# Kernel tuning notes

Hardware: AMD Instinct MI355X
Metric: run time of the kernel (lower is better)

## Reference

```python
import jax, jax.numpy as jnp
import numpy as np

N_NODES = 100_000
N_EDGES = 1_600_000
NFEAT = 16          # nfeature_dim
HID = 128           # hidden_dim
K = 3               # TAGConv hops in pretrained convs
N_LAYERS = 4        # pretrained n_gnn_layers (1 in->hid + 3 hid->hid)
OUT_DIM = 1


def _gcn_norm(edge_index, n):
    # PyG TAGConv: symmetric gcn_norm WITHOUT self-loops (k=0 term covers self).
    row, col = edge_index[0], edge_index[1]
    deg = jax.ops.segment_sum(jnp.ones((edge_index.shape[1],), jnp.float32), col, num_segments=n)
    dis = jnp.where(deg > 0, jax.lax.rsqrt(jnp.maximum(deg, 1.0)), 0.0)
    return dis[row] * dis[col]


def _tagconv(x, row, col, norm, ws, b, n):
    # out = sum_k (A_hat^k x) W_k + b ; ws: [K+1, in, out]
    out = x @ ws[0]
    h = x
    for k in range(1, ws.shape[0]):
        h = jax.ops.segment_sum(h[row] * norm[:, None], col, num_segments=n)
        out = out + h @ ws[k]
    return out + b


def setup_inputs() -> dict:
    key = jax.random.key(0)
    ks = jax.random.split(key, 10)
    x = jax.random.normal(ks[0], (N_NODES, NFEAT + 1), jnp.float32)
    edge_index = jax.random.randint(ks[1], (2, N_EDGES), 0, N_NODES, dtype=jnp.int64)
    # featureEmbedding: TAGConv(17 -> 16, K=1) -> 2 weight mats + bias
    fe_ws = jax.random.normal(ks[2], (2, NFEAT + 1, NFEAT), jnp.float32) * (NFEAT + 1) ** -0.5
    fe_b = jnp.zeros((NFEAT,), jnp.float32)
    # convs[0]: TAGConv(16 -> 128, K=3)
    conv0_ws = jax.random.normal(ks[3], (K + 1, NFEAT, HID), jnp.float32) * NFEAT ** -0.5
    conv0_b = jnp.zeros((HID,), jnp.float32)
    # convs[1..3]: TAGConv(128 -> 128, K=3), stacked
    conv_ws = jax.random.normal(ks[4], (N_LAYERS - 1, K + 1, HID, HID), jnp.float32) * HID ** -0.5
    conv_b = jnp.zeros((N_LAYERS - 1, HID), jnp.float32)
    fc_w = jax.random.normal(ks[5], (HID, OUT_DIM), jnp.float32) * HID ** -0.5
    fc_b = jnp.zeros((OUT_DIM,), jnp.float32)
    return {"x": x, "edge_index": edge_index, "fe_ws": fe_ws, "fe_b": fe_b,
            "conv0_ws": conv0_ws, "conv0_b": conv0_b,
            "conv_ws": conv_ws, "conv_b": conv_b, "fc_w": fc_w, "fc_b": fc_b}


def reference(x, edge_index, fe_ws, fe_b, conv0_ws, conv0_b, conv_ws, conv_b, fc_w, fc_b):
    n = x.shape[0]
    row, col = edge_index[0], edge_index[1]
    norm = _gcn_norm(edge_index, n)
    # featureEmbedding (K=1)
    h = _tagconv(x, row, col, norm, fe_ws, fe_b, n)
    # convs[0..n-2] with dropout (eval-mode identity) + ReLU
    h = _tagconv(h, row, col, norm, conv0_ws, conv0_b, n)
    h = jax.nn.relu(h)
    for i in range(conv_ws.shape[0] - 1):
        h = _tagconv(h, row, col, norm, conv_ws[i], conv_b[i], n)
        h = jax.nn.relu(h)
    # last conv: no dropout/relu
    h = _tagconv(h, row, col, norm, conv_ws[-1], conv_b[-1], n)
    return h @ fc_w + fc_b
```

## Files before the change

### kernel.cpp

```cpp
#include <hip/hip_runtime.h>

#define NN 100000
#define NE 1600000
#define SCAN_B 98
#define NB 782
#define SUBCAP 512
#define MAXB 4096

typedef _Float16 half8 __attribute__((ext_vector_type(8)));
typedef float f32x4 __attribute__((ext_vector_type(4)));
struct h2s { _Float16 x, y; };
struct h4s { _Float16 a, b, c, d; };

__global__ void k_deg(const int* __restrict__ col, int* __restrict__ degi) {
  int e = blockIdx.x * blockDim.x + threadIdx.x;
  if (e < NE) atomicAdd(&degi[col[e]], 1);
}

__global__ void k_dis(const int* __restrict__ degi, float* __restrict__ dis) {
  int i = blockIdx.x * blockDim.x + threadIdx.x;
  if (i < NN) {
    int d = degi[i];
    dis[i] = d > 0 ? rsqrtf((float)d) : 0.0f;
  }
}

__global__ void k_scan1(const int* __restrict__ degi, int* __restrict__ bsum) {
  __shared__ int red[256];
  int t = threadIdx.x;
  int base = blockIdx.x * 1024 + t * 4;
  int s = 0;
#pragma unroll
  for (int u = 0; u < 4; ++u) {
    int i = base + u;
    if (i < NN) s += degi[i];
  }
  red[t] = s;
  __syncthreads();
  for (int o = 128; o; o >>= 1) {
    if (t < o) red[t] += red[t + o];
    __syncthreads();
  }
  if (t == 0) bsum[blockIdx.x] = red[0];
}

__global__ void k_scan2(const int* __restrict__ bsum, int* __restrict__ boff,
                        int* __restrict__ off) {
  __shared__ int sh[128];
  int t = threadIdx.x;
  int v = (t < SCAN_B) ? bsum[t] : 0;
  sh[t] = v;
  __syncthreads();
  for (int o = 1; o < 128; o <<= 1) {
    int u = (t >= o) ? sh[t - o] : 0;
    __syncthreads();
    sh[t] += u;
    __syncthreads();
  }
  if (t < SCAN_B) boff[t] = sh[t] - v;
  if (t == 127) off[NN] = sh[127];
}

__global__ void k_scan3(const int* __restrict__ degi, const int* __restrict__ boff,
                        int* __restrict__ off) {
  __shared__ int red[256];
  int t = threadIdx.x;
  int base = blockIdx.x * 1024 + t * 4;
  int d[4];
  int s = 0;
#pragma unroll
  for (int u = 0; u < 4; ++u) {
    int i = base + u;
    d[u] = (i < NN) ? degi[i] : 0;
    s += d[u];
  }
  red[t] = s;
  __syncthreads();
  for (int o = 1; o < 256; o <<= 1) {
    int u2 = (t >= o) ? red[t - o] : 0;
    __syncthreads();
    red[t] += u2;
    __syncthreads();
  }
  int pre = red[t] - s + boff[blockIdx.x];
#pragma unroll
  for (int u = 0; u < 4; ++u) {
    int i = base + u;
    if (i < NN) {
      off[i] = pre;
      pre += d[u];
    }
  }
}

__global__ void k_bscatter(const int* __restrict__ row, const int* __restrict__ col,
                           int* __restrict__ bcur, unsigned* __restrict__ pk2) {
  int e = blockIdx.x * blockDim.x + threadIdx.x;
  int x = blockIdx.x & 7;
  if (e < NE) {
    int c = col[e];
    int cell = ((c >> 7) << 3) | x;
    int slot = atomicAdd(&bcur[cell * 16], 1);
    slot = min(slot, SUBCAP - 1);
    pk2[(size_t)cell * SUBCAP + slot] = (unsigned)row[e] | ((unsigned)(c & 127) << 17);
  }
}

__global__ __launch_bounds__(256) void k_bsort(const unsigned* __restrict__ pk2,
                                               const int* __restrict__ bcur,
                                               const int* __restrict__ off,
                                               const float* __restrict__ dis,
                                               int* __restrict__ src,
                                               _Float16* __restrict__ wh) {
  __shared__ unsigned epk[MAXB];
  __shared__ int cnt[128];
  __shared__ int sc[128];
  __shared__ int cur[128];
  __shared__ float sdis[128];
  __shared__ int soff[9];
  int b = blockIdx.x;
  int n0 = b << 7;
  int gb = off[n0];
  int t = threadIdx.x;
  if (t == 0) {
    int acc = 0;
#pragma unroll
    for (int x = 0; x < 8; ++x) {
      soff[x] = acc;
      acc += min(bcur[((b << 3) | x) * 16], SUBCAP);
    }
    soff[8] = acc;
  }
  if (t < 128) {
    cnt[t] = 0;
    sdis[t] = (n0 + t < NN) ? dis[n0 + t] : 0.f;
  }
  __syncthreads();
  int m = soff[8];
#pragma unroll
  for (int x = 0; x < 8; ++x) {
    int c0 = soff[x], c1 = soff[x + 1];
    const unsigned* seg = &pk2[(size_t)((b << 3) | x) * SUBCAP];
    for (int i = c0 + t; i < c1; i += 256) epk[i] = seg[i - c0];
  }
  __syncthreads();
  for (int i = t; i < m; i += 256) atomicAdd(&cnt[epk[i] >> 17], 1);
  __syncthreads();
  if (t < 128) sc[t] = cnt[t];
  __syncthreads();
  for (int o = 1; o < 128; o <<= 1) {
    int u = (t < 128 && t >= o) ? sc[t - o] : 0;
    __syncthreads();
    if (t < 128) sc[t] += u;
    __syncthreads();
  }
  if (t < 128) cur[t] = sc[t] - cnt[t];
  __syncthreads();
  for (int i = t; i < m; i += 256) {
    unsigned p = epk[i];
    int c = (int)(p >> 17);
    int r = (int)(p & 0x1FFFFu);
    int pos = gb + atomicAdd(&cur[c], 1);
    src[pos] = r;
    wh[pos] = (_Float16)(dis[r] * sdis[c]);
  }
}

__global__ void k_wprep(const float* __restrict__ cw, _Float16* __restrict__ wt) {
  int i = blockIdx.x * 256 + threadIdx.x;
  if (i < 12 * 16384) {
    int mat = i >> 14;
    int rem = i & 16383;
    int k = rem >> 7;
    int n = rem & 127;
    wt[(mat << 14) | (n << 7) | k] = (_Float16)cw[i];
  }
}

__global__ void k_uprep(const float* __restrict__ cw, const float* __restrict__ cb,
                        const float* __restrict__ fcw, const float* __restrict__ fcb,
                        float* __restrict__ uvec, float* __restrict__ cval) {
  int i = blockIdx.x * 256 + threadIdx.x;
  if (i < 512) {
    int s = i >> 7, k = i & 127;
    const float* W = cw + (size_t)(8 + s) * 16384 + k * 128;
    float acc = 0.f;
    for (int n = 0; n < 128; ++n) acc += W[n] * fcw[n];
    uvec[i] = acc;
  }
  if (i == 512) {
    float acc = 0.f;
    for (int n = 0; n < 128; ++n) acc += cb[2 * 128 + n] * fcw[n];
    *cval = acc + fcb[0];
  }
}

__global__ void k_prop16h(const h2s* __restrict__ h, const int* __restrict__ off,
                          const int* __restrict__ src, const _Float16* __restrict__ wh,
                          h2s* __restrict__ out) {
  int t = threadIdx.x;
  int node = blockIdx.x * 8 + (t >> 3);
  int f = t & 7;
  int b = off[node], e = off[node + 1];
  float ax = 0.f, ay = 0.f;
  int j = b;
  for (; j + 2 <= e; j += 2) {
    int s0 = src[j], s1 = src[j + 1];
    float w0 = (float)wh[j], w1 = (float)wh[j + 1];
    h2s v0 = h[s0 * 8 + f];
    h2s v1 = h[s1 * 8 + f];
    ax = fmaf((float)v0.x, w0, fmaf((float)v1.x, w1, ax));
    ay = fmaf((float)v0.y, w0, fmaf((float)v1.y, w1, ay));
  }
  if (j < e) {
    int s = src[j];
    float w = (float)wh[j];
    h2s v = h[s * 8 + f];
    ax = fmaf((float)v.x, w, ax);
    ay = fmaf((float)v.y, w, ay);
  }
  h2s o;
  o.x = (_Float16)ax;
  o.y = (_Float16)ay;
  unsigned bits;
  __builtin_memcpy(&bits, &o, 4);
  __builtin_nontemporal_store(bits, (unsigned*)&out[node * 8 + f]);
}

__global__ void k_prop128h(const h2s* __restrict__ h, const int* __restrict__ off,
                           const int* __restrict__ src, const _Float16* __restrict__ wh,
                           h2s* __restrict__ out) {
  int node = blockIdx.x;
  int t = threadIdx.x;
  int b = off[node], e = off[node + 1];
  float ax = 0.f, ay = 0.f;
  int j = b;
  for (; j + 8 <= e; j += 8) {
    h2s v[8];
    float w[8];
#pragma unroll
    for (int u = 0; u < 8; ++u) {
      v[u] = h[src[j + u] * 64 + t];
      w[u] = (float)wh[j + u];
    }
#pragma unroll
    for (int u = 0; u < 8; ++u) {
      ax = fmaf((float)v[u].x, w[u], ax);
      ay = fmaf((float)v[u].y, w[u], ay);
    }
  }
  for (; j < e; ++j) {
    int s = src[j];
    float w = (float)wh[j];
    h2s v = h[s * 64 + t];
    ax = fmaf((float)v.x, w, ax);
    ay = fmaf((float)v.y, w, ay);
  }
  h2s o;
  o.x = (_Float16)ax;
  o.y = (_Float16)ay;
  unsigned bits;
  __builtin_memcpy(&bits, &o, 4);
  __builtin_nontemporal_store(bits, (unsigned*)&out[node * 64 + t]);
}

template <bool RELU>
__global__ __launch_bounds__(256) void k_tag4_mfma(
    const _Float16* __restrict__ A0, const _Float16* __restrict__ A1,
    const _Float16* __restrict__ A2, const _Float16* __restrict__ A3,
    const _Float16* __restrict__ Wt, const float* __restrict__ bias,
    _Float16* __restrict__ out) {
  __shared__ _Float16 Wl[16384];
  int tid = threadIdx.x;
  int wid = tid >> 6;
  int lane = tid & 63;
  int r = lane & 15, kg = lane >> 4;
  int m0 = blockIdx.x * 128 + wid * 32;
  int row0 = min(m0 + r, NN - 1);
  int row1 = min(m0 + 16 + r, NN - 1);
  f32x4 acc0[8] = {}, acc1[8] = {};
  const _Float16* As[4] = {A0, A1, A2, A3};
#pragma unroll
  for (int s = 0; s < 4; ++s) {
    const float4* Wg = (const float4*)(Wt + (s << 14));
    __syncthreads();
#pragma unroll
    for (int u = 0; u < 8; ++u) {
      int g = tid + u * 256;
      int sg = g ^ ((g >> 4) & 7);
      *(float4*)((char*)Wl + g * 16) = Wg[sg];
    }
    __syncthreads();
    const _Float16* A = As[s];
    half8 a0[4], a1[4];
#pragma unroll
    for (int kc = 0; kc < 4; ++kc) {
      int kbase = kc * 32 + kg * 8;
      a0[kc] = *(const half8*)&A[(size_t)row0 * 128 + kbase];
      a1[kc] = *(const half8*)&A[(size_t)row1 * 128 + kbase];
    }
#pragma unroll
    for (int kc = 0; kc < 4; ++kc) {
      int kb2 = (kc * 32 + kg * 8) * 2;
#pragma unroll
      for (int nb = 0; nb < 8; ++nb) {
        int n = nb * 16 + r;
        int ba = ((n << 8) + kb2) ^ ((n & 7) << 4);
        half8 b = *(const half8*)((const char*)Wl + ba);
        acc0[nb] = __builtin_amdgcn_mfma_f32_16x16x32_f16(a0[kc], b, acc0[nb], 0, 0, 0);
        acc1[nb] = __builtin_amdgcn_mfma_f32_16x16x32_f16(a1[kc], b, acc1[nb], 0, 0, 0);
      }
    }
  }
  int ccol = lane & 15;
#pragma unroll
  for (int h = 0; h < 2; ++h) {
    int crow0 = m0 + h * 16 + kg * 4;
#pragma unroll
    for (int nb = 0; nb < 8; ++nb) {
      int col = nb * 16 + ccol;
      float bv = bias[col];
      const f32x4& av = h ? acc1[nb] : acc0[nb];
#pragma unroll
      for (int e = 0; e < 4; ++e) {
        float v = av[e] + bv;
        if (RELU) v = fmaxf(v, 0.f);
        int rr = crow0 + e;
        if (rr < NN) out[(size_t)rr * 128 + col] = (_Float16)v;
      }
    }
  }
}

__global__ void k_tagfc(const _Float16* __restrict__ A0, const _Float16* __restrict__ A1,
                        const _Float16* __restrict__ A2, const _Float16* __restrict__ A3,
                        const float* __restrict__ uvec, const float* __restrict__ cval,
                        float* __restrict__ out) {
  int node = blockIdx.x;
  int t = threadIdx.x;
  const h2s* As[4] = {(const h2s*)A0, (const h2s*)A1, (const h2s*)A2, (const h2s*)A3};
  float s = 0.f;
#pragma unroll
  for (int q = 0; q < 4; ++q) {
    h2s v = As[q][(size_t)node * 64 + t];
    float2 u = ((const float2*)(uvec + (q << 7)))[t];
    s = fmaf((float)v.x, u.x, fmaf((float)v.y, u.y, s));
  }
  for (int o = 32; o; o >>= 1) s += __shfl_down(s, o);
  if (t == 0) out[node] = s + *cval;
}

__global__ __launch_bounds__(256) void k_conv0_fused(
    const _Float16* __restrict__ A0, const _Float16* __restrict__ A1,
    const _Float16* __restrict__ A2, const _Float16* __restrict__ A3,
    const float* __restrict__ W , const float* __restrict__ bias,
    _Float16* __restrict__ out) {
  __shared__ float Wl[4 * 16 * 128];
  for (int i = threadIdx.x * 4; i < 4 * 16 * 128; i += 1024)
    *(float4*)&Wl[i] = *(const float4*)&W[i];
  __syncthreads();
  int r0 = blockIdx.x * 32 + (threadIdx.x >> 5) * 4;
  int c0 = (threadIdx.x & 31) * 4;
  float acc[4][4] = {};
  const _Float16* As[4] = {A0, A1, A2, A3};
#pragma unroll
  for (int s = 0; s < 4; ++s) {
    const _Float16* A = As[s];
    const float* Ws = &Wl[s * 2048];
#pragma unroll
    for (int k = 0; k < 16; k += 4) {
      float4 w0 = *(const float4*)&Ws[(k + 0) * 128 + c0];
      float4 w1 = *(const float4*)&Ws[(k + 1) * 128 + c0];
      float4 w2 = *(const float4*)&Ws[(k + 2) * 128 + c0];
      float4 w3 = *(const float4*)&Ws[(k + 3) * 128 + c0];
#pragma unroll
      for (int i = 0; i < 4; ++i) {
        h4s a4 = *(const h4s*)&A[(r0 + i) * 16 + k];
        float ax = (float)a4.a, ay = (float)a4.b, az = (float)a4.c, aw = (float)a4.d;
        acc[i][0] = fmaf(ax, w0.x, fmaf(ay, w1.x, fmaf(az, w2.x, fmaf(aw, w3.x, acc[i][0]))));
        acc[i][1] = fmaf(ax, w0.y, fmaf(ay, w1.y, fmaf(az, w2.y, fmaf(aw, w3.y, acc[i][1]))));
        acc[i][2] = fmaf(ax, w0.z, fmaf(ay, w1.z, fmaf(az, w2.z, fmaf(aw, w3.z, acc[i][2]))));
        acc[i][3] = fmaf(ax, w0.w, fmaf(ay, w1.w, fmaf(az, w2.w, fmaf(aw, w3.w, acc[i][3]))));
      }
    }
  }
#pragma unroll
  for (int i = 0; i < 4; ++i) {
    h4s o;
    o.a = (_Float16)fmaxf(acc[i][0] + bias[c0 + 0], 0.f);
    o.b = (_Float16)fmaxf(acc[i][1] + bias[c0 + 1], 0.f);
    o.c = (_Float16)fmaxf(acc[i][2] + bias[c0 + 2], 0.f);
    o.d = (_Float16)fmaxf(acc[i][3] + bias[c0 + 3], 0.f);
    *(h4s*)&out[(size_t)(r0 + i) * 128 + c0] = o;
  }
}

template <int IN, bool ACCUM, bool BIAS>
__global__ void k_mm16h(const float* __restrict__ A, const float* __restrict__ W,
                        const float* __restrict__ bias, _Float16* __restrict__ C) {
  __shared__ float Wl[IN * 16];
  for (int i = threadIdx.x; i < IN * 16; i += 256) Wl[i] = W[i];
  __syncthreads();
  int r = blockIdx.x * 16 + (threadIdx.x >> 4);
  int c = threadIdx.x & 15;
  float acc = 0.f;
  for (int k = 0; k < IN; ++k) acc += A[r * IN + k] * Wl[k * 16 + c];
  int idx = r * 16 + c;
  if (BIAS) acc += bias[c];
  if (ACCUM) acc += (float)C[idx];
  C[idx] = (_Float16)acc;
}

extern "C" void kernel_launch(void* const* d_in, const int* in_sizes, int n_in,
                              void* d_out, int out_size, void* d_ws, size_t ws_size,
                              hipStream_t stream) {
  const float* x = (const float*)d_in[0];
  const int* ei = (const int*)d_in[1];
  const float* fe_ws = (const float*)d_in[2];
  const float* fe_b = (const float*)d_in[3];
  const float* c0_ws = (const float*)d_in[4];
  const float* c0_b = (const float*)d_in[5];
  const float* cw = (const float*)d_in[6];
  const float* cb = (const float*)d_in[7];
  const float* fcw = (const float*)d_in[8];
  const float* fcb = (const float*)d_in[9];
  float* out = (float*)d_out;

  const int* row = ei;
  const int* colv = ei + NE;

  char* wp = (char*)d_ws;
  auto alloc = [&](size_t bytes) {
    char* p = wp;
    wp += (bytes + 511) & ~(size_t)511;
    return p;
  };
  int* degi = (int*)alloc(NN * 4);
  int* off = (int*)alloc((NN + 1) * 4);
  int* bsum = (int*)alloc(SCAN_B * 4);
  int* boff = (int*)alloc(SCAN_B * 4);
  int* bcur = (int*)alloc((size_t)NB * 8 * 16 * 4);
  float* dis = (float*)alloc(NN * 4);
  int* src = (int*)alloc((size_t)NE * 4);
  unsigned* pk2 = (unsigned*)alloc((size_t)NB * 8 * SUBCAP * 4);
  _Float16* wh = (_Float16*)alloc((size_t)NE * 2);
  _Float16* wsT = (_Float16*)alloc((size_t)12 * 16384 * 2);
  float* uvec = (float*)alloc(512 * 4);
  float* cval = (float*)alloc(4);
  _Float16* y1h = (_Float16*)alloc((size_t)NN * 16 * 2);
  _Float16* h16 = (_Float16*)alloc((size_t)NN * 16 * 2);
  _Float16* p16b = (_Float16*)alloc((size_t)NN * 16 * 2);
  _Float16* p16c = (_Float16*)alloc((size_t)NN * 16 * 2);
  _Float16* p16d = (_Float16*)alloc((size_t)NN * 16 * 2);
  _Float16* H0 = (_Float16*)alloc((size_t)NN * 128 * 2);
  _Float16* H1 = (_Float16*)alloc((size_t)NN * 128 * 2);
  _Float16* T1 = (_Float16*)alloc((size_t)NN * 128 * 2);
  _Float16* T2 = (_Float16*)alloc((size_t)NN * 128 * 2);
  _Float16* T3 = (_Float16*)alloc((size_t)NN * 128 * 2);

  hipMemsetAsync(degi, 0, NN * 4, stream);
  hipMemsetAsync(bcur, 0, (size_t)NB * 8 * 16 * 4, stream);
  k_deg<<<(NE + 255) / 256, 256, 0, stream>>>(colv, degi);
  k_dis<<<(NN + 255) / 256, 256, 0, stream>>>(degi, dis);
  k_scan1<<<SCAN_B, 256, 0, stream>>>(degi, bsum);
  k_scan2<<<1, 128, 0, stream>>>(bsum, boff, off);
  k_scan3<<<SCAN_B, 256, 0, stream>>>(degi, boff, off);
  k_bscatter<<<(NE + 255) / 256, 256, 0, stream>>>(row, colv, bcur, pk2);
  k_bsort<<<NB, 256, 0, stream>>>(pk2, bcur, off, dis, src, wh);
  k_wprep<<<768, 256, 0, stream>>>(cw, wsT);
  k_uprep<<<3, 256, 0, stream>>>(cw, cb, fcw, fcb, uvec, cval);

  k_mm16h<17, false, false><<<NN / 16, 256, 0, stream>>>(x, fe_ws + 17 * 16, nullptr, y1h);
  k_prop16h<<<NN / 8, 64, 0, stream>>>((const h2s*)y1h, off, src, wh, (h2s*)h16);
  k_mm16h<17, true, true><<<NN / 16, 256, 0, stream>>>(x, fe_ws, fe_b, h16);

  k_prop16h<<<NN / 8, 64, 0, stream>>>((const h2s*)h16, off, src, wh, (h2s*)p16b);
  k_prop16h<<<NN / 8, 64, 0, stream>>>((const h2s*)p16b, off, src, wh, (h2s*)p16c);
  k_prop16h<<<NN / 8, 64, 0, stream>>>((const h2s*)p16c, off, src, wh, (h2s*)p16d);
  k_conv0_fused<<<NN / 32, 256, 0, stream>>>(h16, p16b, p16c, p16d, c0_ws, c0_b, H0);

  _Float16* hin = H0;
  _Float16* hout = H1;
  int mgrid = (NN + 127) / 128;
  for (int l = 0; l < 2; ++l) {
    k_prop128h<<<NN, 64, 0, stream>>>((const h2s*)hin, off, src, wh, (h2s*)T1);
    k_prop128h<<<NN, 64, 0, stream>>>((const h2s*)T1, off, src, wh, (h2s*)T2);
    k_prop128h<<<NN, 64, 0, stream>>>((const h2s*)T2, off, src, wh, (h2s*)T3);
    const _Float16* Wl = wsT + (size_t)l * 4 * 16384;
    const float* bl = cb + l * 128;
    k_tag4_mfma<true><<<mgrid, 256, 0, stream>>>(hin, T1, T2, T3, Wl, bl, hout);
    _Float16* t = hin; hin = hout; hout = t;
  }

  k_prop128h<<<NN, 64, 0, stream>>>((const h2s*)hin, off, src, wh, (h2s*)T1);
  k_prop128h<<<NN, 64, 0, stream>>>((const h2s*)T1, off, src, wh, (h2s*)T2);
  k_prop128h<<<NN, 64, 0, stream>>>((const h2s*)T2, off, src, wh, (h2s*)T3);
  k_tagfc<<<NN, 64, 0, stream>>>(hin, T1, T2, T3, uvec, cval, out);
}
```

Measured before the change: 942.3 us.

## Pack edge source and weight into one 64-bit record, shuffle-broadcast in propagation

Replaces the separate src (int) and fp16 weight arrays with one 64-bit array holding the source index and an fp32 weight. In the 128-wide propagation kernel, each group of 8 lanes loads one packed record and broadcasts it with a shuffle, instead of every lane reading the index and weight separately. That kernel also moves from one 64-thread block per node to four nodes per 256-thread block, and bscatter uses a nontemporal store. This cuts scalar index loads and block-launch overhead, at the cost of more edge bytes (8 instead of 6 per edge) and added shuffle instructions.

Result: slower. 1.067 ms (+13.2%).

```diff
diff --git a/kernel.cpp b/kernel.cpp
--- a/kernel.cpp
+++ b/kernel.cpp
@@ -11,6 +11,12 @@
 typedef float f32x4 __attribute__((ext_vector_type(4)));
 struct h2s { _Float16 x, y; };
 struct h4s { _Float16 a, b, c, d; };
+
+static __device__ __forceinline__ void unpack_pair(long pv, int& s, float& w) {
+  s = (int)(unsigned int)(pv & 0xffffffffL);
+  int wi = (int)(pv >> 32);
+  __builtin_memcpy(&w, &wi, 4);
+}
 
 __global__ void k_deg(const int* __restrict__ col, int* __restrict__ degi) {
   int e = blockIdx.x * blockDim.x + threadIdx.x;
@@ -102,7 +108,8 @@
     int cell = ((c >> 7) << 3) | x;
     int slot = atomicAdd(&bcur[cell * 16], 1);
     slot = min(slot, SUBCAP - 1);
-    pk2[(size_t)cell * SUBCAP + slot] = (unsigned)row[e] | ((unsigned)(c & 127) << 17);
+    unsigned v = (unsigned)row[e] | ((unsigned)(c & 127) << 17);
+    __builtin_nontemporal_store(v, &pk2[(size_t)cell * SUBCAP + slot]);
   }
 }
 
@@ -110,8 +117,7 @@
                                                const int* __restrict__ bcur,
                                                const int* __restrict__ off,
                                                const float* __restrict__ dis,
-                                               int* __restrict__ src,
-                                               _Float16* __restrict__ wh) {
+                                               long* __restrict__ E) {
   __shared__ unsigned epk[MAXB];
   __shared__ int cnt[128];
   __shared__ int sc[128];
@@ -161,8 +167,10 @@
     int c = (int)(p >> 17);
     int r = (int)(p & 0x1FFFFu);
     int pos = gb + atomicAdd(&cur[c], 1);
-    src[pos] = r;
-    wh[pos] = (_Float16)(dis[r] * sdis[c]);
+    float w = dis[r] * sdis[c];
+    int wi;
+    __builtin_memcpy(&wi, &w, 4);
+    E[pos] = (long)(unsigned int)r | ((long)wi << 32);
   }
 }
 
@@ -196,8 +204,7 @@
 }
 
 __global__ void k_prop16h(const h2s* __restrict__ h, const int* __restrict__ off,
-                          const int* __restrict__ src, const _Float16* __restrict__ wh,
-                          h2s* __restrict__ out) {
+                          const long* __restrict__ E, h2s* __restrict__ out) {
   int t = threadIdx.x;
   int node = blockIdx.x * 8 + (t >> 3);
   int f = t & 7;
@@ -205,16 +212,19 @@
   float ax = 0.f, ay = 0.f;
   int j = b;
   for (; j + 2 <= e; j += 2) {
-    int s0 = src[j], s1 = src[j + 1];
-    float w0 = (float)wh[j], w1 = (float)wh[j + 1];
+    int s0, s1;
+    float w0, w1;
+    unpack_pair(E[j], s0, w0);
+    unpack_pair(E[j + 1], s1, w1);
     h2s v0 = h[s0 * 8 + f];
     h2s v1 = h[s1 * 8 + f];
     ax = fmaf((float)v0.x, w0, fmaf((float)v1.x, w1, ax));
     ay = fmaf((float)v0.y, w0, fmaf((float)v1.y, w1, ay));
   }
   if (j < e) {
-    int s = src[j];
-    float w = (float)wh[j];
+    int s;
+    float w;
+    unpack_pair(E[j], s, w);
     h2s v = h[s * 8 + f];
     ax = fmaf((float)v.x, w, ax);
     ay = fmaf((float)v.y, w, ay);
@@ -227,21 +237,25 @@
   __builtin_nontemporal_store(bits, (unsigned*)&out[node * 8 + f]);
 }
 
-__global__ void k_prop128h(const h2s* __restrict__ h, const int* __restrict__ off,
-                           const int* __restrict__ src, const _Float16* __restrict__ wh,
-                           h2s* __restrict__ out) {
-  int node = blockIdx.x;
-  int t = threadIdx.x;
+__global__ __launch_bounds__(256) void k_prop128h(const h2s* __restrict__ h,
+                                                  const int* __restrict__ off,
+                                                  const long* __restrict__ E,
+                                                  h2s* __restrict__ out) {
+  int node = blockIdx.x * 4 + (threadIdx.x >> 6);
+  int t = threadIdx.x & 63;
   int b = off[node], e = off[node + 1];
   float ax = 0.f, ay = 0.f;
   int j = b;
   for (; j + 8 <= e; j += 8) {
+    long pv = E[j + (t & 7)];
     h2s v[8];
     float w[8];
 #pragma unroll
     for (int u = 0; u < 8; ++u) {
-      v[u] = h[src[j + u] * 64 + t];
-      w[u] = (float)wh[j + u];
+      long p = __shfl(pv, u, 8);
+      int s;
+      unpack_pair(p, s, w[u]);
+      v[u] = h[s * 64 + t];
     }
 #pragma unroll
     for (int u = 0; u < 8; ++u) {
@@ -250,8 +264,9 @@
     }
   }
   for (; j < e; ++j) {
-    int s = src[j];
-    float w = (float)wh[j];
+    int s;
+    float w;
+    unpack_pair(E[j], s, w);
     h2s v = h[s * 64 + t];
     ax = fmaf((float)v.x, w, ax);
     ay = fmaf((float)v.y, w, ay);
@@ -441,9 +456,8 @@
   int* boff = (int*)alloc(SCAN_B * 4);
   int* bcur = (int*)alloc((size_t)NB * 8 * 16 * 4);
   float* dis = (float*)alloc(NN * 4);
-  int* src = (int*)alloc((size_t)NE * 4);
+  long* E = (long*)alloc((size_t)NE * 8);
   unsigned* pk2 = (unsigned*)alloc((size_t)NB * 8 * SUBCAP * 4);
-  _Float16* wh = (_Float16*)alloc((size_t)NE * 2);
   _Float16* wsT = (_Float16*)alloc((size_t)12 * 16384 * 2);
   float* uvec = (float*)alloc(512 * 4);
   float* cval = (float*)alloc(4);
@@ -466,34 +480,35 @@
   k_scan2<<<1, 128, 0, stream>>>(bsum, boff, off);
   k_scan3<<<SCAN_B, 256, 0, stream>>>(degi, boff, off);
   k_bscatter<<<(NE + 255) / 256, 256, 0, stream>>>(row, colv, bcur, pk2);
-  k_bsort<<<NB, 256, 0, stream>>>(pk2, bcur, off, dis, src, wh);
+  k_bsort<<<NB, 256, 0, stream>>>(pk2, bcur, off, dis, E);
   k_wprep<<<768, 256, 0, stream>>>(cw, wsT);
   k_uprep<<<3, 256, 0, stream>>>(cw, cb, fcw, fcb, uvec, cval);
 
   k_mm16h<17, false, false><<<NN / 16, 256, 0, stream>>>(x, fe_ws + 17 * 16, nullptr, y1h);
-  k_prop16h<<<NN / 8, 64, 0, stream>>>((const h2s*)y1h, off, src, wh, (h2s*)h16);
+  k_prop16h<<<NN / 8, 64, 0, stream>>>((const h2s*)y1h, off, E, (h2s*)h16);
   k_mm16h<17, true, true><<<NN / 16, 256, 0, stream>>>(x, fe_ws, fe_b, h16);
 
-  k_prop16h<<<NN / 8, 64, 0, stream>>>((const h2s*)h16, off, src, wh, (h2s*)p16b);
-  k_prop16h<<<NN / 8, 64, 0, stream>>>((const h2s*)p16b, off, src, wh, (h2s*)p16c);
-  k_prop16h<<<NN / 8, 64, 0, stream>>>((const h2s*)p16c, off, src, wh, (h2s*)p16d);
+  k_prop16h<<<NN / 8, 64, 0, stream>>>((const h2s*)h16, off, E, (h2s*)p16b);
+  k_prop16h<<<NN / 8, 64, 0, stream>>>((const h2s*)p16b, off, E, (h2s*)p16c);
+  k_prop16h<<<NN / 8, 64, 0, stream>>>((const h2s*)p16c, off, E, (h2s*)p16d);
   k_conv0_fused<<<NN / 32, 256, 0, stream>>>(h16, p16b, p16c, p16d, c0_ws, c0_b, H0);
 
   _Float16* hin = H0;
   _Float16* hout = H1;
   int mgrid = (NN + 127) / 128;
+  int pgrid = NN / 4;
   for (int l = 0; l < 2; ++l) {
-    k_prop128h<<<NN, 64, 0, stream>>>((const h2s*)hin, off, src, wh, (h2s*)T1);
-    k_prop128h<<<NN, 64, 0, stream>>>((const h2s*)T1, off, src, wh, (h2s*)T2);
-    k_prop128h<<<NN, 64, 0, stream>>>((const h2s*)T2, off, src, wh, (h2s*)T3);
+    k_prop128h<<<pgrid, 256, 0, stream>>>((const h2s*)hin, off, E, (h2s*)T1);
+    k_prop128h<<<pgrid, 256, 0, stream>>>((const h2s*)T1, off, E, (h2s*)T2);
+    k_prop128h<<<pgrid, 256, 0, stream>>>((const h2s*)T2, off, E, (h2s*)T3);
     const _Float16* Wl = wsT + (size_t)l * 4 * 16384;
     const float* bl = cb + l * 128;
     k_tag4_mfma<true><<<mgrid, 256, 0, stream>>>(hin, T1, T2, T3, Wl, bl, hout);
     _Float16* t = hin; hin = hout; hout = t;
   }
 
-  k_prop128h<<<NN, 64, 0, stream>>>((const h2s*)hin, off, src, wh, (h2s*)T1);
-  k_prop128h<<<NN, 64, 0, stream>>>((const h2s*)T1, off, src, wh, (h2s*)T2);
-  k_prop128h<<<NN, 64, 0, stream>>>((const h2s*)T2, off, src, wh, (h2s*)T3);
+  k_prop128h<<<pgrid, 256, 0, stream>>>((const h2s*)hin, off, E, (h2s*)T1);
+  k_prop128h<<<pgrid, 256, 0, stream>>>((const h2s*)T1, off, E, (h2s*)T2);
+  k_prop128h<<<pgrid, 256, 0, stream>>>((const h2s*)T2, off, E, (h2s*)T3);
   k_tagfc<<<NN, 64, 0, stream>>>(hin, T1, T2, T3, uvec, cval, out);
 }
```
